# Kernel optimization log

Hardware: AMD Instinct MI355X
Metric: run time of the kernel (lower is better)

The kernel has to match this reference:

```python
import jax, jax.numpy as jnp
import numpy as np

EMB = 512
QKV = 512
H = 8      # num_heads
PH = 8     # num_pheads
HD = QKV // H
PHD = QKV // PH


def _make_params(key):
    names = ['Wi', 'Wip', 'Wic', 'Wq', 'Wpq', 'Wk', 'Wpk', 'Wv', 'Wpv', 'Wo', 'Wop']
    ks = jax.random.split(key, len(names))
    p = {}
    for n, k in zip(names, ks):
        din = EMB if n in ('Wi', 'Wip', 'Wic') else QKV
        dout = EMB if n in ('Wo', 'Wop') else QKV
        p[n] = jax.random.normal(k, (din, dout), jnp.float32) * 0.02
        p['b' + n[1:]] = jnp.zeros((dout,), jnp.float32)
    return p


def setup_inputs() -> dict:
    key = jax.random.key(0)
    kq, kp, kc, kw = jax.random.split(key, 4)
    B, S, P = 16, 4096, 64
    inp = {
        'query': jax.random.normal(kq, (B, S, EMB), jnp.float32),
        'pquery': jax.random.normal(kp, (B, P, EMB), jnp.float32),
        'context': jax.random.normal(kc, (B, S, EMB), jnp.float32),
    }
    inp.update(_make_params(kw))
    return inp


def reference(query, pquery, context,
              Wi, bi, Wip, bip, Wic, bic,
              Wq, bq, Wpq, bpq, Wk, bk, Wpk, bpk,
              Wv, bv, Wpv, bpv, Wo, bo, Wop, bop):
    # Dropout layers act as identity (eval mode / deterministic reference).
    B, S, _ = query.shape
    P = pquery.shape[1]

    q_in = query @ Wi + bi        # (B,S,QKV)
    pq_in = pquery @ Wip + bip    # (B,P,QKV)
    c_in = context @ Wic + bic    # (B,S,QKV)

    # --- pack stage: pquery attends over context -> p_context ---
    pq = ((pq_in @ Wpq + bpq) * (PHD ** -0.5)).reshape(B, P, PH, PHD)
    pk = (c_in @ Wpk + bpk).reshape(B, S, PH, PHD)
    pv = (c_in @ Wpv + bpv).reshape(B, S, PH, PHD)
    # dropout before softmax in original; identity here
    pattn = jax.nn.softmax(jnp.einsum('bphd,bshd->bhps', pq, pk), axis=-1)
    pc = jnp.einsum('bhps,bshd->bphd', pattn, pv).reshape(B, P, QKV)

    # --- unpack stage: query attends over p_context ---
    q = ((q_in @ Wq + bq) * (HD ** -0.5)).reshape(B, S, H, HD)
    k = (pc @ Wk + bk).reshape(B, P, H, HD)
    v = (pc @ Wv + bv).reshape(B, P, H, HD)
    aw = jax.nn.softmax(jnp.einsum('bshd,bphd->bhsp', q, k), axis=-1)  # (B,H,S,P)
    attn = jnp.einsum('bhsp,bphd->bshd', aw, v).reshape(B, S, QKV)
    attn = attn @ Wo + bo           # (B,S,EMB)
    pc_out = pc @ Wop + bop         # (B,P,EMB)

    # torch returns attn_weights as (S, B*H, P) when batch_first
    aw_t = jnp.transpose(aw.reshape(B * H, S, P), (1, 0, 2))
    return attn, pc_out, aw_t
```

## Files before the change

kernel.cpp:

```cpp
#include <hip/hip_runtime.h>


typedef __bf16 bf16x8 __attribute__((ext_vector_type(8)));
typedef float f32x4 __attribute__((ext_vector_type(4)));
typedef unsigned short u16x8 __attribute__((ext_vector_type(8)));
typedef unsigned short u16x4 __attribute__((ext_vector_type(4)));

#define MFMA16(a, b, c) __builtin_amdgcn_mfma_f32_16x16x32_bf16((a), (b), (c), 0, 0, 0)

__device__ __forceinline__ unsigned short f2bf_bits(float f) {
  unsigned int u = __float_as_uint(f);
  u += 0x7fffu + ((u >> 16) & 1u);
  return (unsigned short)(u >> 16);
}

__device__ __forceinline__ void gload16(const void* g, void* l) {
  __builtin_amdgcn_global_load_lds(
      (const __attribute__((address_space(1))) void*)g,
      (__attribute__((address_space(3))) void*)l, 16, 0, 0);
}

struct Ptr8 { const float* p[8]; };

__global__ __launch_bounds__(256) void prep_kernel(
    Ptr8 srcs, unsigned short* __restrict__ WT,
    const float* bi, const float* bip, const float* bic,
    const float* Wq, const float* Wpq, const float* Wpk, const float* Wpv,
    const float* bq, const float* bpq, const float* bpk, const float* bpv,
    float* __restrict__ bias_out) {
  const int t = threadIdx.x;
  if (blockIdx.z < 8) {
    const float* __restrict__ W = srcs.p[blockIdx.z];
    unsigned short* __restrict__ O = WT + (size_t)blockIdx.z * 262144;
    __shared__ float tile[32][33];
    const int tr = blockIdx.x * 32, tc = blockIdx.y * 32;
    {
      const int r = t >> 3, c4 = (t & 7) * 4;
      const float4 v = *reinterpret_cast<const float4*>(&W[(size_t)(tr + r) * 512 + tc + c4]);
      tile[r][c4 + 0] = v.x; tile[r][c4 + 1] = v.y; tile[r][c4 + 2] = v.z; tile[r][c4 + 3] = v.w;
    }
    __syncthreads();
    {
      const int n = t >> 3, k4 = (t & 7) * 4;
      u16x4 o;
#pragma unroll
      for (int j = 0; j < 4; j++) o[j] = f2bf_bits(tile[k4 + j][n]);
      *reinterpret_cast<u16x4*>(&O[(size_t)(tc + n) * 512 + tr + k4]) = o;
    }
  } else {
    const int idx = blockIdx.y * 16 + blockIdx.x;
    if (idx >= 8) return;
    const int y = idx >> 1;
    const float* bin  = (y == 0) ? bi : (y == 1) ? bip : bic;
    const float* W    = (y == 0) ? Wq : (y == 1) ? Wpq : (y == 2) ? Wpk : Wpv;
    const float* bout = (y == 0) ? bq : (y == 1) ? bpq : (y == 2) ? bpk : bpv;
    const float scale = (y < 2) ? 0.125f : 1.0f;
    const int n = (idx & 1) * 256 + t;
    float s = 0.f;
    for (int k = 0; k < 512; k++) s += bin[k] * W[(size_t)k * 512 + n];
    bias_out[y * 512 + n] = (s + bout[n]) * scale;
  }
}

__global__ __launch_bounds__(256) void gemm_wcomb(
    const float* __restrict__ Wi, const float* __restrict__ Wip,
    const float* __restrict__ Wic, const unsigned short* __restrict__ WTbase,
    unsigned short* __restrict__ outbase) {
  const int z = blockIdx.z;
  const float* __restrict__ A = (z == 0) ? Wi : (z == 1) ? Wip : Wic;
  const unsigned short* __restrict__ BT = WTbase + (size_t)z * 262144;
  unsigned short* __restrict__ out = outbase + (size_t)z * 262144;
  const float scale = (z < 2) ? 0.125f : 1.0f;

  __shared__ __align__(16) unsigned short As[128 * 72];
  __shared__ __align__(16) unsigned short Bs[128 * 72];
  const int t = threadIdx.x;
  const int w = t >> 6, l = t & 63, li = l & 15, lg = l >> 4;
  const int wm = w >> 1, wn = w & 1;
  const int m0 = blockIdx.x * 128, n0 = blockIdx.y * 128;

  f32x4 acc[4][4] = {};

  for (int kt = 0; kt < 512; kt += 64) {
#pragma unroll
    for (int i = 0; i < 8; i++) {
      const int row = i * 16 + (t >> 4), k = (t & 15) * 4;
      const float4 v = *reinterpret_cast<const float4*>(&A[(size_t)(m0 + row) * 512 + kt + k]);
      u16x4 o;
      o[0] = f2bf_bits(v.x); o[1] = f2bf_bits(v.y);
      o[2] = f2bf_bits(v.z); o[3] = f2bf_bits(v.w);
      *reinterpret_cast<u16x4*>(&As[row * 72 + k]) = o;
    }
#pragma unroll
    for (int i = 0; i < 4; i++) {
      const int row = i * 32 + (t >> 3), k = (t & 7) * 8;
      const u16x8 v = *reinterpret_cast<const u16x8*>(&BT[(size_t)(n0 + row) * 512 + kt + k]);
      *reinterpret_cast<u16x8*>(&Bs[row * 72 + k]) = v;
    }
    __syncthreads();
#pragma unroll
    for (int kk = 0; kk < 2; kk++) {
      bf16x8 a[4], b[4];
#pragma unroll
      for (int mf = 0; mf < 4; mf++)
        a[mf] = *reinterpret_cast<const bf16x8*>(&As[(wm * 64 + mf * 16 + li) * 72 + kk * 32 + lg * 8]);
#pragma unroll
      for (int nf = 0; nf < 4; nf++)
        b[nf] = *reinterpret_cast<const bf16x8*>(&Bs[(wn * 64 + nf * 16 + li) * 72 + kk * 32 + lg * 8]);
#pragma unroll
      for (int mf = 0; mf < 4; mf++)
#pragma unroll
        for (int nf = 0; nf < 4; nf++)
          acc[mf][nf] = MFMA16(a[mf], b[nf], acc[mf][nf]);
    }
    __syncthreads();
  }
  const int lg4 = lg * 4;
#pragma unroll
  for (int nf = 0; nf < 4; nf++) {
    const int col = n0 + wn * 64 + nf * 16 + li;
#pragma unroll
    for (int mf = 0; mf < 4; mf++) {
      const int row = m0 + wm * 64 + mf * 16 + lg4;
#pragma unroll
      for (int r = 0; r < 4; r++)
        out[(size_t)col * 512 + row + r] = f2bf_bits(acc[mf][nf][r] * scale);
    }
  }
}

#define WAITV(n)                                            \
  {                                                         \
    asm volatile("s_waitcnt vmcnt(" #n ")" ::: "memory");   \
    __builtin_amdgcn_sched_barrier(0);                      \
  }
#define BAR3()                                              \
  {                                                         \
    __builtin_amdgcn_s_barrier();                           \
    __builtin_amdgcn_sched_barrier(0);                      \
  }

__device__ __forceinline__ void gemm3pf_body(
    const float* __restrict__ A, const unsigned short* __restrict__ BT,
    const float* __restrict__ bias, unsigned short* out, int Ntiles, int ldc,
    int wg) {
  __shared__ __align__(16) float Asf[2][128 * 32];
  __shared__ __align__(16) unsigned short Bs[2][128 * 32];
  const int t = threadIdx.x;
  const int w = t >> 6, l = t & 63, li = l & 15, lg = l >> 4;
  const int wm = w >> 1, wn = w & 1;
  const int m0 = (wg / Ntiles) * 128, n0 = (wg % Ntiles) * 128;

  f32x4 acc[4][4] = {};
  const int arow_ = t >> 3, aslot_ = t & 7;
  const int brow_ = t >> 2, bslot_ = t & 3;

#define STAGEF(tile, bb)                                                       \
  {                                                                            \
    const int kt = (tile) * 32;                                                \
    _Pragma("unroll") for (int i = 0; i < 4; i++) {                            \
      const int row = i * 32 + arow_;                                          \
      const int gs = (aslot_ ^ (row & 7)) * 4;                                 \
      gload16(&A[(size_t)(m0 + row) * 512 + kt + gs],                          \
              &Asf[bb][(i * 256 + t) * 4]);                                    \
    }                                                                          \
    _Pragma("unroll") for (int i = 0; i < 2; i++) {                            \
      const int row = i * 64 + brow_;                                          \
      const int gs = (bslot_ ^ ((row >> 1) & 3)) * 8;                          \
      gload16(&BT[(size_t)(n0 + row) * 512 + kt + gs],                         \
              &Bs[bb][(i * 256 + t) * 8]);                                     \
    }                                                                          \
  }

#define COMPUTEF(bb)                                                           \
  {                                                                            \
    bf16x8 a[4], b[4];                                                         \
    _Pragma("unroll") for (int mf = 0; mf < 4; mf++) {                         \
      const int r = wm * 64 + mf * 16 + li;                                    \
      const f32x4 lo = *reinterpret_cast<const f32x4*>(                        \
          &Asf[bb][r * 32 + (((2 * lg) ^ (r & 7)) * 4)]);                      \
      const f32x4 hi = *reinterpret_cast<const f32x4*>(                        \
          &Asf[bb][r * 32 + (((2 * lg + 1) ^ (r & 7)) * 4)]);                  \
      bf16x8 v;                                                                \
      _Pragma("unroll") for (int j = 0; j < 4; j++) {                          \
        v[j] = (__bf16)lo[j];                                                  \
        v[j + 4] = (__bf16)hi[j];                                              \
      }                                                                        \
      a[mf] = v;                                                               \
    }                                                                          \
    _Pragma("unroll") for (int nf = 0; nf < 4; nf++) {                         \
      const int r = wn * 64 + nf * 16 + li;                                    \
      b[nf] = *reinterpret_cast<const bf16x8*>(                                \
          &Bs[bb][r * 32 + ((lg ^ ((r >> 1) & 3)) * 8)]);                      \
    }                                                                          \
    _Pragma("unroll") for (int mf = 0; mf < 4; mf++)                           \
        _Pragma("unroll") for (int nf = 0; nf < 4; nf++)                       \
            acc[mf][nf] = MFMA16(a[mf], b[nf], acc[mf][nf]);                   \
  }

  STAGEF(0, 0);
  STAGEF(1, 1);

#pragma unroll 1
  for (int tt = 0; tt < 14; ++tt) {
    WAITV(6);
    BAR3();
    COMPUTEF(tt & 1);
    BAR3();
    STAGEF(tt + 2, tt & 1);
  }
  WAITV(6); BAR3(); COMPUTEF(0); BAR3();
  WAITV(0); BAR3(); COMPUTEF(1);

#undef STAGEF
#undef COMPUTEF

  const int lg4 = lg * 4;
#pragma unroll
  for (int nf = 0; nf < 4; nf++) {
    const int col = n0 + wn * 64 + nf * 16 + li;
    const float bv = bias[col];
#pragma unroll
    for (int mf = 0; mf < 4; mf++) {
      const int row = m0 + wm * 64 + mf * 16 + lg4;
#pragma unroll
      for (int r = 0; r < 4; r++)
        out[(size_t)(row + r) * ldc + col] = f2bf_bits(acc[mf][nf][r] + bv);
    }
  }
}

__global__ __launch_bounds__(256, 3) void gemm3pf_qpkv(
    const float* query, const float* context, const float* pquery,
    const unsigned short* WqeT, const unsigned short* WpkveT,
    const unsigned short* WpqeT, const float* bqe, const float* bpkve,
    const float* bpqe, unsigned short* q_buf, unsigned short* pkv_buf,
    unsigned short* pq_buf) {
  const int q8 = gridDim.x >> 3;
  int wg = ((int)blockIdx.x & 7) * q8 + ((int)blockIdx.x >> 3);
  const float* A;
  const unsigned short* BT;
  const float* bias;
  unsigned short* out;
  int Ntiles, ldc;
  if (wg < 2048) {
    A = query; BT = WqeT; bias = bqe; out = q_buf; Ntiles = 4; ldc = 512;
  } else if (wg < 6144) {
    wg -= 2048; A = context; BT = WpkveT; bias = bpkve; out = pkv_buf;
    Ntiles = 8; ldc = 1024;
  } else {
    wg -= 6144; A = pquery; BT = WpqeT; bias = bpqe; out = pq_buf;
    Ntiles = 4; ldc = 512;
  }
  gemm3pf_body(A, BT, bias, out, Ntiles, ldc, wg);
}

template <int OUTF32>
__device__ __forceinline__ void gemm3p_body(
    const unsigned short* __restrict__ A, const unsigned short* __restrict__ BT,
    const float* __restrict__ bias, void* out, int Ntiles, int ldc, int wg) {
  __shared__ __align__(16) unsigned short As[3][128 * 32];
  __shared__ __align__(16) unsigned short Bs[3][128 * 32];
  const int t = threadIdx.x;
  const int w = t >> 6, l = t & 63, li = l & 15, lg = l >> 4;
  const int wm = w >> 1, wn = w & 1;
  const int m0 = (wg / Ntiles) * 128, n0 = (wg % Ntiles) * 128;

  f32x4 acc[4][4] = {};
  const int srow = t >> 2, sslot = t & 3;

#define STAGE3(tile)                                                           \
  {                                                                            \
    const int bb = (tile) % 3;                                                 \
    const int kt = (tile) * 32;                                                \
    _Pragma("unroll") for (int i = 0; i < 2; i++) {                            \
      const int row = i * 64 + srow;                                           \
      const int gs = (sslot ^ ((row >> 1) & 3)) * 8;                           \
      gload16(&A[(size_t)(m0 + row) * 512 + kt + gs], &As[bb][(i * 256 + t) * 8]); \
    }                                                                          \
    _Pragma("unroll") for (int i = 0; i < 2; i++) {                            \
      const int row = i * 64 + srow;                                           \
      const int gs = (sslot ^ ((row >> 1) & 3)) * 8;                           \
      gload16(&BT[(size_t)(n0 + row) * 512 + kt + gs], &Bs[bb][(i * 256 + t) * 8]); \
    }                                                                          \
  }

#define COMPUTE3(tile)                                                         \
  {                                                                            \
    const int bb = (tile) % 3;                                                 \
    bf16x8 a[4], b[4];                                                         \
    _Pragma("unroll") for (int mf = 0; mf < 4; mf++) {                         \
      const int r = wm * 64 + mf * 16 + li;                                    \
      a[mf] = *reinterpret_cast<const bf16x8*>(                                \
          &As[bb][r * 32 + ((lg ^ ((r >> 1) & 3)) * 8)]);                      \
    }                                                                          \
    _Pragma("unroll") for (int nf = 0; nf < 4; nf++) {                         \
      const int r = wn * 64 + nf * 16 + li;                                    \
      b[nf] = *reinterpret_cast<const bf16x8*>(                                \
          &Bs[bb][r * 32 + ((lg ^ ((r >> 1) & 3)) * 8)]);                      \
    }                                                                          \
    _Pragma("unroll") for (int mf = 0; mf < 4; mf++)                           \
        _Pragma("unroll") for (int nf = 0; nf < 4; nf++)                       \
            acc[mf][nf] = MFMA16(a[mf], b[nf], acc[mf][nf]);                   \
  }

  STAGE3(0);
  STAGE3(1);
  STAGE3(2);

#pragma unroll 1
  for (int tt = 0; tt < 13; ++tt) {
    WAITV(8);
    BAR3();
    COMPUTE3(tt);
    BAR3();
    STAGE3(tt + 3);
  }
  WAITV(8); BAR3(); COMPUTE3(13); BAR3();
  WAITV(4); BAR3(); COMPUTE3(14); BAR3();
  WAITV(0); BAR3(); COMPUTE3(15);

#undef STAGE3
#undef COMPUTE3

  const int lg4 = lg * 4;
#pragma unroll
  for (int nf = 0; nf < 4; nf++) {
    const int col = n0 + wn * 64 + nf * 16 + li;
    const float bv = bias[col];
#pragma unroll
    for (int mf = 0; mf < 4; mf++) {
      const int row = m0 + wm * 64 + mf * 16 + lg4;
      if constexpr (OUTF32) {
        float* o = (float*)out;
#pragma unroll
        for (int r = 0; r < 4; r++)
          o[(size_t)(row + r) * ldc + col] = acc[mf][nf][r] + bv;
      } else {
        unsigned short* o = (unsigned short*)out;
#pragma unroll
        for (int r = 0; r < 4; r++)
          o[(size_t)(row + r) * ldc + col] = f2bf_bits(acc[mf][nf][r] + bv);
      }
    }
  }
}

__global__ __launch_bounds__(256, 3) void gemm3p_final(
    const unsigned short* A, const unsigned short* BT, const float* bias,
    float* out) {
  const int q8 = gridDim.x >> 3;
  const int wg = ((int)blockIdx.x & 7) * q8 + ((int)blockIdx.x >> 3);
  gemm3p_body<1>(A, BT, bias, out, 4, 512, wg);
}

__global__ __launch_bounds__(256) void gemm_kvpc(
    const unsigned short* __restrict__ A, const unsigned short* __restrict__ BT,
    const float* __restrict__ bias0, const float* __restrict__ bias1,
    const float* __restrict__ bias2, unsigned short* out0, unsigned short* out1,
    float* out2, int Ntiles) {
  __shared__ __align__(16) unsigned short As[128 * 64];
  __shared__ __align__(16) unsigned short Bs[128 * 64];
  const int t = threadIdx.x;
  const int w = t >> 6, l = t & 63, li = l & 15, lg = l >> 4;
  const int wm = w >> 1, wn = w & 1;
  const int K = 512;
  const int m0 = (blockIdx.x / Ntiles) * 128, n0 = (blockIdx.x % Ntiles) * 128;

  f32x4 acc[4][4] = {};
  const int sr = t >> 3, sslot = t & 7;

  for (int kt = 0; kt < K; kt += 64) {
#pragma unroll
    for (int i = 0; i < 4; i++) {
      const int row = i * 32 + sr;
      const int gs = (sslot ^ (row & 7)) * 8;
      gload16(&A[(size_t)(m0 + row) * K + kt + gs], &As[(i * 256 + t) * 8]);
      gload16(&BT[(size_t)(n0 + row) * K + kt + gs], &Bs[(i * 256 + t) * 8]);
    }
    __syncthreads();
#pragma unroll
    for (int kk = 0; kk < 2; kk++) {
      bf16x8 a[4], b[4];
#pragma unroll
      for (int mf = 0; mf < 4; mf++) {
        const int r = wm * 64 + mf * 16 + li;
        a[mf] = *reinterpret_cast<const bf16x8*>(&As[r * 64 + (((kk * 4 + lg) ^ (r & 7)) * 8)]);
      }
#pragma unroll
      for (int nf = 0; nf < 4; nf++) {
        const int r = wn * 64 + nf * 16 + li;
        b[nf] = *reinterpret_cast<const bf16x8*>(&Bs[r * 64 + (((kk * 4 + lg) ^ (r & 7)) * 8)]);
      }
#pragma unroll
      for (int mf = 0; mf < 4; mf++)
#pragma unroll
        for (int nf = 0; nf < 4; nf++)
          acc[mf][nf] = MFMA16(a[mf], b[nf], acc[mf][nf]);
    }
    __syncthreads();
  }

  const int lg4 = lg * 4;
#pragma unroll
  for (int nf = 0; nf < 4; nf++) {
    const int col = n0 + wn * 64 + nf * 16 + li;
    if (col < 512) {
      const float bv = bias0[col];
#pragma unroll
      for (int mf = 0; mf < 4; mf++) {
        const int row = m0 + wm * 64 + mf * 16 + lg4;
#pragma unroll
        for (int r = 0; r < 4; r++)
          out0[(size_t)(row + r) * 512 + col] = f2bf_bits(acc[mf][nf][r] + bv);
      }
    } else if (col < 1024) {
      const float bv = bias1[col - 512];
#pragma unroll
      for (int mf = 0; mf < 4; mf++) {
        const int row = m0 + wm * 64 + mf * 16 + lg4;
#pragma unroll
        for (int r = 0; r < 4; r++)
          out1[(size_t)(row + r) * 512 + col - 512] = f2bf_bits(acc[mf][nf][r] + bv);
      }
    } else {
      const float bv = bias2[col - 1024];
#pragma unroll
      for (int mf = 0; mf < 4; mf++) {
        const int row = m0 + wm * 64 + mf * 16 + lg4;
#pragma unroll
        for (int r = 0; r < 4; r++)
          out2[(size_t)(row + r) * 512 + col - 1024] = acc[mf][nf][r] + bv;
      }
    }
  }
}

__global__ __launch_bounds__(256) void pack_attn(
    const unsigned short* __restrict__ pq_buf,
    const unsigned short* __restrict__ pkv_buf, float* __restrict__ partial) {
  __shared__ __align__(16) unsigned short pkL[64 * 72];
  __shared__ __align__(16) unsigned short pvT[64 * 72];
  __shared__ __align__(16) unsigned short prL[4 * 16 * 72];
  const int t = threadIdx.x, w = t >> 6, l = t & 63, li = l & 15, lg = l >> 4;
  const int bh = blockIdx.x, b = bh >> 3, h = bh & 7;
  const int sb = blockIdx.y * 512;

  bf16x8 aq[2];
  {
    const size_t base = ((size_t)(b * 64 + w * 16 + li)) * 512 + h * 64;
    aq[0] = *reinterpret_cast<const bf16x8*>(&pq_buf[base + lg * 8]);
    aq[1] = *reinterpret_cast<const bf16x8*>(&pq_buf[base + 32 + lg * 8]);
  }

  f32x4 acc[4] = {};
  float lsum[4] = {};

  for (int st = 0; st < 8; st++) {
    const int s0 = sb + st * 64;
#pragma unroll
    for (int i = 0; i < 2; i++) {
      const int row = i * 32 + (t >> 3), c = (t & 7) * 8;
      const u16x8 v = *reinterpret_cast<const u16x8*>(
          &pkv_buf[((size_t)(b * 4096 + s0 + row)) * 1024 + h * 64 + c]);
      *reinterpret_cast<u16x8*>(&pkL[row * 72 + c]) = v;
    }
    {
      const int rp = t >> 3, c = (t & 7) * 8;
      const size_t base = ((size_t)(b * 4096 + s0 + 2 * rp)) * 1024 + 512 + h * 64 + c;
      const u16x8 u0 = *reinterpret_cast<const u16x8*>(&pkv_buf[base]);
      const u16x8 u1 = *reinterpret_cast<const u16x8*>(&pkv_buf[base + 1024]);
#pragma unroll
      for (int j = 0; j < 8; j++) {
        const int val = ((int)u0[j] & 0xffff) | ((int)u1[j] << 16);
        *reinterpret_cast<int*>(&pvT[(c + j) * 72 + 2 * rp]) = val;
      }
    }
    __syncthreads();
    f32x4 sc[4] = {};
#pragma unroll
    for (int nf = 0; nf < 4; nf++) {
#pragma unroll
      for (int kk = 0; kk < 2; kk++) {
        const bf16x8 bk = *reinterpret_cast<const bf16x8*>(
            &pkL[(nf * 16 + li) * 72 + kk * 32 + lg * 8]);
        sc[nf] = MFMA16(aq[kk], bk, sc[nf]);
      }
    }
#pragma unroll
    for (int nf = 0; nf < 4; nf++) {
#pragma unroll
      for (int r = 0; r < 4; r++) {
        const float e = __expf(sc[nf][r]);
        lsum[r] += e;
        prL[(w * 16 + lg * 4 + r) * 72 + nf * 16 + li] = f2bf_bits(e);
      }
    }
#pragma unroll
    for (int kk = 0; kk < 2; kk++) {
      const bf16x8 ap = *reinterpret_cast<const bf16x8*>(
          &prL[(w * 16 + li) * 72 + kk * 32 + lg * 8]);
#pragma unroll
      for (int nf = 0; nf < 4; nf++) {
        const bf16x8 bv = *reinterpret_cast<const bf16x8*>(
            &pvT[(nf * 16 + li) * 72 + kk * 32 + lg * 8]);
        acc[nf] = MFMA16(ap, bv, acc[nf]);
      }
    }
    __syncthreads();
  }

#pragma unroll
  for (int m = 1; m < 16; m <<= 1)
#pragma unroll
    for (int r = 0; r < 4; r++) lsum[r] += __shfl_xor(lsum[r], m);

  const size_t pbase = ((size_t)(bh * 8 + blockIdx.y)) * 4160;
#pragma unroll
  for (int nf = 0; nf < 4; nf++)
#pragma unroll
    for (int r = 0; r < 4; r++)
      partial[pbase + (size_t)(w * 16 + lg * 4 + r) * 64 + nf * 16 + li] = acc[nf][r];
  if (li == 0)
#pragma unroll
    for (int r = 0; r < 4; r++) partial[pbase + 4096 + w * 16 + lg * 4 + r] = lsum[r];
}

__global__ __launch_bounds__(256) void pack_combine(const float* __restrict__ partial,
                                                    unsigned short* __restrict__ pc_buf) {
  const int bh = blockIdx.x, b = bh >> 3, h = bh & 7;
  const int t = threadIdx.x;
#pragma unroll
  for (int e = 0; e < 16; e++) {
    const int idx = e * 256 + t;
    const int p = idx >> 6, d = idx & 63;
    float s = 0.f, den = 0.f;
#pragma unroll
    for (int c = 0; c < 8; c++) {
      const float* pb = &partial[((size_t)(bh * 8 + c)) * 4160];
      s += pb[idx];
      den += pb[4096 + p];
    }
    pc_buf[((size_t)(b * 64 + p)) * 512 + h * 64 + d] = f2bf_bits(s / den);
  }
}

__global__ __launch_bounds__(256) void unpack_attn(
    const unsigned short* q_in, const unsigned short* __restrict__ k_buf,
    const unsigned short* __restrict__ v_buf, float* __restrict__ aw_out,
    unsigned short* attnh_out) {
  __shared__ __align__(16) unsigned short kL[64 * 72];
  __shared__ __align__(16) unsigned short vT[64 * 72];
  __shared__ __align__(16) unsigned short prL[4 * 64 * 72];
  const int t = threadIdx.x, w = t >> 6, l = t & 63, li = l & 15, lg = l >> 4;
  const int bh = blockIdx.y, b = bh >> 3, h = bh & 7;
  const int sbase = blockIdx.x * 256 + w * 64;

#pragma unroll
  for (int i = 0; i < 2; i++) {
    const int p = i * 32 + (t >> 3), c = (t & 7) * 8;
    const u16x8 v = *reinterpret_cast<const u16x8*>(
        &k_buf[((size_t)(b * 64 + p)) * 512 + h * 64 + c]);
    *reinterpret_cast<u16x8*>(&kL[p * 72 + c]) = v;
  }
  {
    const int rp = t >> 3, c = (t & 7) * 8;
    const size_t base = ((size_t)(b * 64 + 2 * rp)) * 512 + h * 64 + c;
    const u16x8 u0 = *reinterpret_cast<const u16x8*>(&v_buf[base]);
    const u16x8 u1 = *reinterpret_cast<const u16x8*>(&v_buf[base + 512]);
#pragma unroll
    for (int j = 0; j < 8; j++) {
      const int val = ((int)u0[j] & 0xffff) | ((int)u1[j] << 16);
      *reinterpret_cast<int*>(&vT[(c + j) * 72 + 2 * rp]) = val;
    }
  }
  bf16x8 aq[4][2];
#pragma unroll
  for (int mf = 0; mf < 4; mf++) {
    const size_t base = ((size_t)(b * 4096 + sbase + mf * 16 + li)) * 512 + h * 64;
    aq[mf][0] = *reinterpret_cast<const bf16x8*>(&q_in[base + lg * 8]);
    aq[mf][1] = *reinterpret_cast<const bf16x8*>(&q_in[base + 32 + lg * 8]);
  }
  __syncthreads();

  f32x4 sc[4][4] = {};
#pragma unroll
  for (int kk = 0; kk < 2; kk++)
#pragma unroll
    for (int nf = 0; nf < 4; nf++) {
      const bf16x8 bk = *reinterpret_cast<const bf16x8*>(
          &kL[(nf * 16 + li) * 72 + kk * 32 + lg * 8]);
#pragma unroll
      for (int mf = 0; mf < 4; mf++) sc[mf][nf] = MFMA16(aq[mf][kk], bk, sc[mf][nf]);
    }

#pragma unroll
  for (int mf = 0; mf < 4; mf++) {
#pragma unroll
    for (int r = 0; r < 4; r++) {
      float e[4];
      float rs = 0.f;
#pragma unroll
      for (int nf = 0; nf < 4; nf++) {
        e[nf] = __expf(sc[mf][nf][r]);
        rs += e[nf];
      }
#pragma unroll
      for (int m = 1; m < 16; m <<= 1) rs += __shfl_xor(rs, m);
      const float inv = 1.0f / rs;
      const int srow = sbase + mf * 16 + lg * 4 + r;
#pragma unroll
      for (int nf = 0; nf < 4; nf++) {
        const float pr = e[nf] * inv;
        aw_out[(size_t)srow * 8192 + bh * 64 + nf * 16 + li] = pr;
        prL[(w * 64 + mf * 16 + lg * 4 + r) * 72 + nf * 16 + li] = f2bf_bits(pr);
      }
    }
  }

  f32x4 acc[4][4] = {};
#pragma unroll
  for (int kk = 0; kk < 2; kk++)
#pragma unroll
    for (int mf = 0; mf < 4; mf++) {
      const bf16x8 ap = *reinterpret_cast<const bf16x8*>(
          &prL[(w * 64 + mf * 16 + li) * 72 + kk * 32 + lg * 8]);
#pragma unroll
      for (int nf = 0; nf < 4; nf++) {
        const bf16x8 bv = *reinterpret_cast<const bf16x8*>(
            &vT[(nf * 16 + li) * 72 + kk * 32 + lg * 8]);
        acc[mf][nf] = MFMA16(ap, bv, acc[mf][nf]);
      }
    }
#pragma unroll
  for (int mf = 0; mf < 4; mf++)
#pragma unroll
    for (int nf = 0; nf < 4; nf++)
#pragma unroll
      for (int r = 0; r < 4; r++)
        attnh_out[((size_t)(b * 4096 + sbase + mf * 16 + lg * 4 + r)) * 512 + h * 64 +
                  nf * 16 + li] = f2bf_bits(acc[mf][nf][r]);
}

extern "C" void kernel_launch(void* const* d_in, const int* in_sizes, int n_in,
                              void* d_out, int out_size, void* d_ws, size_t ws_size,
                              hipStream_t stream) {
  (void)in_sizes; (void)n_in; (void)out_size; (void)ws_size;

  const float* query   = (const float*)d_in[0];
  const float* pquery  = (const float*)d_in[1];
  const float* context = (const float*)d_in[2];
  const float* Wi  = (const float*)d_in[3];  const float* bi  = (const float*)d_in[4];
  const float* Wip = (const float*)d_in[5];  const float* bip = (const float*)d_in[6];
  const float* Wic = (const float*)d_in[7];  const float* bic = (const float*)d_in[8];
  const float* Wq  = (const float*)d_in[9];  const float* bq  = (const float*)d_in[10];
  const float* Wpq = (const float*)d_in[11]; const float* bpq = (const float*)d_in[12];
  const float* Wk  = (const float*)d_in[13]; const float* bk  = (const float*)d_in[14];
  const float* Wpk = (const float*)d_in[15]; const float* bpk = (const float*)d_in[16];
  const float* Wv  = (const float*)d_in[17]; const float* bv  = (const float*)d_in[18];
  const float* Wpv = (const float*)d_in[19]; const float* bpv = (const float*)d_in[20];
  const float* Wo  = (const float*)d_in[21]; const float* bo  = (const float*)d_in[22];
  const float* Wop = (const float*)d_in[23]; const float* bop = (const float*)d_in[24];

  char* ws = (char*)d_ws;
  unsigned short* WT     = (unsigned short*)(ws);
  unsigned short* WqeT   = (unsigned short*)(ws + 4u * 1024 * 1024);
  unsigned short* WpqeT  = WqeT + 512 * 512;
  unsigned short* WpkveT = WpqeT + 512 * 512;
  float* bqe   = (float*)(WpkveT + (size_t)1024 * 512);
  float* bpqe  = bqe + 512;
  float* bpkve = bpqe + 512;
  unsigned short* q_buf   = (unsigned short*)(ws + 8u * 1024 * 1024);
  unsigned short* pkv_buf = q_buf + (size_t)65536 * 512;
  unsigned short* pq_buf  = pkv_buf + (size_t)65536 * 1024;
  unsigned short* pc_buf  = pq_buf + (size_t)1024 * 512;
  unsigned short* k_buf   = pc_buf + (size_t)1024 * 512;
  unsigned short* v_buf   = k_buf + (size_t)1024 * 512;
  float* partial = (float*)(v_buf + (size_t)1024 * 512);

  float* out_attn = (float*)d_out;
  float* out_pc   = out_attn + (size_t)16 * 4096 * 512;
  float* out_aw   = out_pc + (size_t)16 * 64 * 512;

  const dim3 blk(256);

  Ptr8 tsrc; tsrc.p[0]=Wq; tsrc.p[1]=Wpq; tsrc.p[2]=Wpk; tsrc.p[3]=Wpv;
  tsrc.p[4]=Wk; tsrc.p[5]=Wv; tsrc.p[6]=Wop; tsrc.p[7]=Wo;
  prep_kernel<<<dim3(16, 16, 9), blk, 0, stream>>>(
      tsrc, WT, bi, bip, bic, Wq, Wpq, Wpk, Wpv, bq, bpq, bpk, bpv, bqe);
  gemm_wcomb<<<dim3(4, 4, 4), blk, 0, stream>>>(Wi, Wip, Wic, WT, WqeT);

  gemm3pf_qpkv<<<dim3(6176), blk, 0, stream>>>(
      query, context, pquery, WqeT, WpkveT, WpqeT, bqe, bpkve, bpqe,
      q_buf, pkv_buf, pq_buf);

  pack_attn<<<dim3(128, 8), blk, 0, stream>>>(pq_buf, pkv_buf, partial);
  pack_combine<<<128, blk, 0, stream>>>(partial, pc_buf);

  gemm_kvpc<<<dim3(96), blk, 0, stream>>>(
      pc_buf, WT + (size_t)4 * 262144, bk, bv, bop, k_buf, v_buf, out_pc, 12);

  unpack_attn<<<dim3(16, 128), blk, 0, stream>>>(q_buf, k_buf, v_buf, out_aw, q_buf);

  gemm3p_final<<<dim3(2048), blk, 0, stream>>>(
      q_buf, WT + (size_t)7 * 262144, bo, out_attn);
}
```

Measured before the change: 507.4 us.

## Convert fp32 A tiles to bf16 in registers before LDS in first GEMM

The large fp32-input GEMM now loads A tiles into registers, converts them to bf16 once, and writes swizzled bf16 into LDS, instead of staging fp32 into LDS via direct global-to-LDS loads and converting on every fragment read. This halves A's LDS footprint and removes redundant per-wave conversions. B gets triple buffering, and occupancy is raised to 4 blocks per CU. In exchange, A loads now pass through VGPRs with register prefetch, which adds register pressure and an extra lgkm wait per iteration.

```diff
diff --git a/kernel.cpp b/kernel.cpp
--- a/kernel.cpp
+++ b/kernel.cpp
@@ -134,59 +134,74 @@
     asm volatile("s_waitcnt vmcnt(" #n ")" ::: "memory");   \
     __builtin_amdgcn_sched_barrier(0);                      \
   }
+#define WAITLGKM()                                          \
+  {                                                         \
+    asm volatile("s_waitcnt lgkmcnt(0)" ::: "memory");      \
+    __builtin_amdgcn_sched_barrier(0);                      \
+  }
 #define BAR3()                                              \
   {                                                         \
     __builtin_amdgcn_s_barrier();                           \
     __builtin_amdgcn_sched_barrier(0);                      \
   }
 
-__device__ __forceinline__ void gemm3pf_body(
+__device__ __forceinline__ void gemm_hyb_body(
     const float* __restrict__ A, const unsigned short* __restrict__ BT,
-    const float* __restrict__ bias, unsigned short* out, int Ntiles, int ldc,
-    int wg) {
-  __shared__ __align__(16) float Asf[2][128 * 32];
-  __shared__ __align__(16) unsigned short Bs[2][128 * 32];
+    const float* __restrict__ bias, unsigned short* __restrict__ out,
+    int Ntiles, int ldc, int wg) {
+  __shared__ __align__(16) unsigned short As[2][128 * 32];
+  __shared__ __align__(16) unsigned short Bs[3][128 * 32];
   const int t = threadIdx.x;
   const int w = t >> 6, l = t & 63, li = l & 15, lg = l >> 4;
   const int wm = w >> 1, wn = w & 1;
   const int m0 = (wg / Ntiles) * 128, n0 = (wg % Ntiles) * 128;
 
   f32x4 acc[4][4] = {};
-  const int arow_ = t >> 3, aslot_ = t & 7;
-  const int brow_ = t >> 2, bslot_ = t & 3;
-
-#define STAGEF(tile, bb)                                                       \
+  float4 ra[2][2];
+  const int rrow = t >> 2;
+  const int slot = (t & 3) ^ ((t >> 3) & 3);
+  const float* aptr = A + (size_t)(m0 + rrow) * 512 + slot * 8;
+
+#define ISSUE_A(kt)                                                            \
   {                                                                            \
+    ra[0][0] = *reinterpret_cast<const float4*>(aptr + (kt));                  \
+    ra[0][1] = *reinterpret_cast<const float4*>(aptr + (kt) + 4);              \
+    ra[1][0] = *reinterpret_cast<const float4*>(aptr + 64 * 512 + (kt));       \
+    ra[1][1] = *reinterpret_cast<const float4*>(aptr + 64 * 512 + (kt) + 4);   \
+  }
+
+#define CVT_WRITE_A(buf)                                                       \
+  {                                                                            \
+    _Pragma("unroll") for (int i = 0; i < 2; i++) {                            \
+      bf16x8 v;                                                                \
+      _Pragma("unroll") for (int j = 0; j < 4; j++) {                          \
+        v[j] = (__bf16)ra[i][0][j];                                            \
+        v[j + 4] = (__bf16)ra[i][1][j];                                        \
+      }                                                                        \
+      *reinterpret_cast<bf16x8*>(&As[buf][(i * 256 + t) * 8]) = v;             \
+    }                                                                          \
+  }
+
+#define STAGE_B(tile)                                                          \
+  {                                                                            \
+    const int bb = (tile) % 3;                                                 \
     const int kt = (tile) * 32;                                                \
-    _Pragma("unroll") for (int i = 0; i < 4; i++) {                            \
-      const int row = i * 32 + arow_;                                          \
-      const int gs = (aslot_ ^ (row & 7)) * 4;                                 \
-      gload16(&A[(size_t)(m0 + row) * 512 + kt + gs],                          \
-              &Asf[bb][(i * 256 + t) * 4]);                                    \
-    }                                                                          \
     _Pragma("unroll") for (int i = 0; i < 2; i++) {                            \
-      const int row = i * 64 + brow_;                                          \
-      const int gs = (bslot_ ^ ((row >> 1) & 3)) * 8;                          \
-      gload16(&BT[(size_t)(n0 + row) * 512 + kt + gs],                         \
+      const int row = i * 64 + rrow;                                           \
+      gload16(&BT[(size_t)(n0 + row) * 512 + kt + slot * 8],                   \
               &Bs[bb][(i * 256 + t) * 8]);                                     \
     }                                                                          \
   }
 
-#define COMPUTEF(bb)                                                           \
+#define COMPUTE(tile)                                                          \
   {                                                                            \
+    const int ab = (tile) & 1;                                                 \
+    const int bb = (tile) % 3;                                                 \
     bf16x8 a[4], b[4];                                                         \
     _Pragma("unroll") for (int mf = 0; mf < 4; mf++) {                         \
       const int r = wm * 64 + mf * 16 + li;                                    \
-      const f32x4 lo = *reinterpret_cast<const f32x4*>(                        \
-          &Asf[bb][r * 32 + (((2 * lg) ^ (r & 7)) * 4)]);                      \
-      const f32x4 hi = *reinterpret_cast<const f32x4*>(                        \
-          &Asf[bb][r * 32 + (((2 * lg + 1) ^ (r & 7)) * 4)]);                  \
-      bf16x8 v;                                                                \
-      _Pragma("unroll") for (int j = 0; j < 4; j++) {                          \
-        v[j] = (__bf16)lo[j];                                                  \
-        v[j + 4] = (__bf16)hi[j];                                              \
-      }                                                                        \
-      a[mf] = v;                                                               \
+      a[mf] = *reinterpret_cast<const bf16x8*>(                                \
+          &As[ab][r * 32 + ((lg ^ ((r >> 1) & 3)) * 8)]);                      \
     }                                                                          \
     _Pragma("unroll") for (int nf = 0; nf < 4; nf++) {                         \
       const int r = wn * 64 + nf * 16 + li;                                    \
@@ -198,22 +213,34 @@
             acc[mf][nf] = MFMA16(a[mf], b[nf], acc[mf][nf]);                   \
   }
 
-  STAGEF(0, 0);
-  STAGEF(1, 1);
+  ISSUE_A(0);
+  STAGE_B(0);
+  STAGE_B(1);
+  WAITV(4);
+  CVT_WRITE_A(0);
+  ISSUE_A(32);
 
 #pragma unroll 1
-  for (int tt = 0; tt < 14; ++tt) {
-    WAITV(6);
+  for (int tt = 0; tt < 15; ++tt) {
+    WAITV(2);
+    CVT_WRITE_A((tt + 1) & 1);
+    if (tt < 14) {
+      ISSUE_A((tt + 2) * 32);
+      STAGE_B(tt + 2);
+    }
+    WAITLGKM();
     BAR3();
-    COMPUTEF(tt & 1);
+    COMPUTE(tt);
     BAR3();
-    STAGEF(tt + 2, tt & 1);
-  }
-  WAITV(6); BAR3(); COMPUTEF(0); BAR3();
-  WAITV(0); BAR3(); COMPUTEF(1);
-
-#undef STAGEF
-#undef COMPUTEF
+  }
+  WAITV(0);
+  BAR3();
+  COMPUTE(15);
+
+#undef ISSUE_A
+#undef CVT_WRITE_A
+#undef STAGE_B
+#undef COMPUTE
 
   const int lg4 = lg * 4;
 #pragma unroll
@@ -230,7 +257,7 @@
   }
 }
 
-__global__ __launch_bounds__(256, 3) void gemm3pf_qpkv(
+__global__ __launch_bounds__(256, 4) void gemm_hyb_qpkv(
     const float* query, const float* context, const float* pquery,
     const unsigned short* WqeT, const unsigned short* WpkveT,
     const unsigned short* WpqeT, const float* bqe, const float* bpkve,
@@ -252,13 +279,13 @@
     wg -= 6144; A = pquery; BT = WpqeT; bias = bpqe; out = pq_buf;
     Ntiles = 4; ldc = 512;
   }
-  gemm3pf_body(A, BT, bias, out, Ntiles, ldc, wg);
-}
-
-template <int OUTF32>
-__device__ __forceinline__ void gemm3p_body(
+  gemm_hyb_body(A, BT, bias, out, Ntiles, ldc, wg);
+}
+
+__device__ __forceinline__ void gemm3p_body_f32out(
     const unsigned short* __restrict__ A, const unsigned short* __restrict__ BT,
-    const float* __restrict__ bias, void* out, int Ntiles, int ldc, int wg) {
+    const float* __restrict__ bias, float* __restrict__ out, int Ntiles,
+    int ldc, int wg) {
   __shared__ __align__(16) unsigned short As[3][128 * 32];
   __shared__ __align__(16) unsigned short Bs[3][128 * 32];
   const int t = threadIdx.x;
@@ -331,17 +358,9 @@
 #pragma unroll
     for (int mf = 0; mf < 4; mf++) {
       const int row = m0 + wm * 64 + mf * 16 + lg4;
-      if constexpr (OUTF32) {
-        float* o = (float*)out;
-#pragma unroll
-        for (int r = 0; r < 4; r++)
-          o[(size_t)(row + r) * ldc + col] = acc[mf][nf][r] + bv;
-      } else {
-        unsigned short* o = (unsigned short*)out;
-#pragma unroll
-        for (int r = 0; r < 4; r++)
-          o[(size_t)(row + r) * ldc + col] = f2bf_bits(acc[mf][nf][r] + bv);
-      }
+#pragma unroll
+      for (int r = 0; r < 4; r++)
+        out[(size_t)(row + r) * ldc + col] = acc[mf][nf][r] + bv;
     }
   }
 }
@@ -351,7 +370,7 @@
     float* out) {
   const int q8 = gridDim.x >> 3;
   const int wg = ((int)blockIdx.x & 7) * q8 + ((int)blockIdx.x >> 3);
-  gemm3p_body<1>(A, BT, bias, out, 4, 512, wg);
+  gemm3p_body_f32out(A, BT, bias, out, 4, 512, wg);
 }
 
 __global__ __launch_bounds__(256) void gemm_kvpc(
@@ -690,7 +709,7 @@
       tsrc, WT, bi, bip, bic, Wq, Wpq, Wpk, Wpv, bq, bpq, bpk, bpv, bqe);
   gemm_wcomb<<<dim3(4, 4, 4), blk, 0, stream>>>(Wi, Wip, Wic, WT, WqeT);
 
-  gemm3pf_qpkv<<<dim3(6176), blk, 0, stream>>>(
+  gemm_hyb_qpkv<<<dim3(6176), blk, 0, stream>>>(
       query, context, pquery, WqeT, WpkveT, WpqeT, bqe, bpkve, bpqe,
       q_buf, pkv_buf, pq_buf);
 
```

Result: no change. 507.3 us (-0.0%).
